# Kernel optimization log

Measured on AMD Instinct MI355X. Metric: run time of the kernel, lower is better.

## Reference

```python
import jax, jax.numpy as jnp
import numpy as np

N_NODES = 100000
FEAT = 256
HID = 256
BATCH = 512
NUM_SAMPLES = [25, 10]  # layer_infos[0].num_samples, layer_infos[1].num_samples


def setup_inputs() -> dict:
    key = jax.random.key(0)
    ks = jax.random.split(key, 7)
    scale = 0.05
    return {
        "features": jax.random.normal(ks[0], (N_NODES, FEAT), dtype=jnp.float32),
        "adj": jax.random.randint(ks[1], (N_NODES, NUM_SAMPLES[0]), 0, N_NODES, dtype=jnp.int32),
        "batch": jax.random.randint(ks[2], (BATCH,), 0, N_NODES, dtype=jnp.int32),
        "W_self_0": jax.random.normal(ks[3], (FEAT, HID), dtype=jnp.float32) * scale,
        "W_neigh_0": jax.random.normal(ks[4], (FEAT, HID), dtype=jnp.float32) * scale,
        "W_self_1": jax.random.normal(ks[5], (HID, HID), dtype=jnp.float32) * scale,
        "W_neigh_1": jax.random.normal(ks[6], (HID, HID), dtype=jnp.float32) * scale,
    }


def reference(features, adj, batch, W_self_0, W_neigh_0, W_self_1, W_neigh_1):
    B = batch.shape[0]
    n_layers = 2
    # --- sample(): reverse-order neighbor expansion (deterministic: first-k slots) ---
    # hop 1 uses layer_infos[-1].num_samples = 10, hop 2 uses layer_infos[0].num_samples = 25
    s1 = adj[batch][:, : NUM_SAMPLES[1]].reshape(-1)  # [B*10]
    s2 = adj[s1][:, : NUM_SAMPLES[0]].reshape(-1)     # [B*250]
    support = [1, NUM_SAMPLES[1], NUM_SAMPLES[1] * NUM_SAMPLES[0]]  # [1, 10, 250]
    # --- gather input features per hop (irregular gather, memory bound) ---
    hidden = [features[batch], features[s1], features[s2]]
    Ws = [(W_self_0, W_neigh_0), (W_self_1, W_neigh_1)]
    for layer in range(n_layers):
        act = jax.nn.relu if layer < n_layers - 1 else (lambda x: x)
        W_s, W_n = Ws[layer]
        next_hidden = []
        for hop in range(n_layers - layer):
            n_smp = NUM_SAMPLES[n_layers - hop - 1]
            self_vecs = hidden[hop]  # [B*support[hop], d]
            neigh = hidden[hop + 1].reshape(B * support[hop], n_smp, -1)
            neigh_mean = neigh.mean(axis=1)  # mean aggregator
            # concat=False -> sum of self and neighbor transforms
            next_hidden.append(act(self_vecs @ W_s + neigh_mean @ W_n))
        hidden = next_hidden
    out = hidden[0]  # [B, HID]
    # GraphSAGE l2-normalizes final embeddings
    norm = jnp.maximum(jnp.linalg.norm(out, axis=1, keepdims=True), 1e-12)
    return out / norm
```

## Files before the change

### kernel.cpp

```cpp
#include <hip/hip_runtime.h>
#include <cstdint>
#include <cstddef>

#define NNODES 100000
#define FEATD  256
#define HIDD   256
#define NBATCH 512
#define FAN1   10
#define FAN2   25
#define NS1    (NBATCH*FAN1)
#define MTOT   (NBATCH+NS1)

typedef __attribute__((ext_vector_type(8))) short short8;
typedef __attribute__((ext_vector_type(4))) float f32x4;

__device__ __forceinline__ unsigned short f2bf(float f) {
    unsigned int u = __float_as_uint(f);
    unsigned int r = (u + 0x7fffu + ((u >> 16) & 1u)) >> 16;
    return (unsigned short)r;
}
__device__ __forceinline__ float bf2f(unsigned short h) {
    return __uint_as_float(((unsigned int)h) << 16);
}

__global__ __launch_bounds__(256) void k_wcvt(
    const float* __restrict__ Ws0, const float* __restrict__ Wn0,
    const float* __restrict__ Ws1, const float* __restrict__ Wn1,
    unsigned short* __restrict__ B0t, unsigned short* __restrict__ B1t) {
    __shared__ unsigned short Ts[64][72];
    const int t     = threadIdx.x;
    const int which = blockIdx.x >> 5;
    const int loc   = blockIdx.x & 31;
    const int kt = loc >> 2, nt = loc & 3;
    const int k0 = kt * 64, n0 = nt * 64;
    const float* W;
    if (which == 0)
        W = (k0 < 256) ? (Ws0 + (size_t)k0 * 256) : (Wn0 + (size_t)(k0 - 256) * 256);
    else
        W = (k0 < 256) ? (Ws1 + (size_t)k0 * 256) : (Wn1 + (size_t)(k0 - 256) * 256);
    unsigned short* Bt = which ? B1t : B0t;
    #pragma unroll
    for (int i = 0; i < 4; ++i) {
        int s  = t + i * 256;
        int kr = s >> 4;
        int c4 = s & 15;
        float4 v = *reinterpret_cast<const float4*>(W + (size_t)kr * 256 + n0 + c4 * 4);
        Ts[c4 * 4 + 0][kr] = f2bf(v.x);
        Ts[c4 * 4 + 1][kr] = f2bf(v.y);
        Ts[c4 * 4 + 2][kr] = f2bf(v.z);
        Ts[c4 * 4 + 3][kr] = f2bf(v.w);
    }
    __syncthreads();
    #pragma unroll
    for (int i = 0; i < 2; ++i) {
        int s  = t + i * 256;
        int nl = s >> 3;
        int k8 = (s & 7) * 8;
        *reinterpret_cast<short8*>(Bt + (size_t)(n0 + nl) * 512 + k0 + k8) =
            *reinterpret_cast<const short8*>(&Ts[nl][k8]);
    }
}

__global__ __launch_bounds__(256, 3) void k_gg0(
    const float* __restrict__ feat, const int* __restrict__ adj,
    const int* __restrict__ batch, const unsigned short* __restrict__ B0t,
    unsigned short* __restrict__ H0, unsigned short* __restrict__ H1) {
    __shared__ __align__(16) unsigned short As[16][520];
    const int t   = threadIdx.x;
    const int wv  = t >> 6;
    const int l   = t & 63;
    const int q   = l >> 4;
    const int m15 = l & 15;
    const int r0  = blockIdx.x * 16;
    const bool isBatch = (r0 < NBATCH);

    #pragma unroll
    for (int i = 0; i < 4; ++i) {
        const int r = wv * 4 + i;
        const int R = r0 + r;
        int node;
        if (isBatch) {
            node = batch[R];
        } else {
            int idx = R - NBATCH;
            int b   = idx / FAN1;
            int j   = idx - b * FAN1;
            node = adj[(size_t)batch[b] * FAN2 + j];
        }
        float4 selfv = *reinterpret_cast<const float4*>(
            feat + (size_t)node * FEATD + l * 4);
        const int* arow = adj + (size_t)node * FAN2;
        int myidx = (l < FAN2) ? arow[l] : 0;
        float4 acc = make_float4(0.f, 0.f, 0.f, 0.f);
        float s;
        if (isBatch) {
            #pragma unroll
            for (int k = 0; k < FAN1; ++k) {
                int nb = __shfl(myidx, k);
                float4 v = *reinterpret_cast<const float4*>(
                    feat + (size_t)nb * FEATD + l * 4);
                acc.x += v.x; acc.y += v.y; acc.z += v.z; acc.w += v.w;
            }
            s = 1.0f / (float)FAN1;
        } else {
            #pragma unroll
            for (int k = 0; k < FAN2; ++k) {
                int nb = __shfl(myidx, k);
                float4 v = *reinterpret_cast<const float4*>(
                    feat + (size_t)nb * FEATD + l * 4);
                acc.x += v.x; acc.y += v.y; acc.z += v.z; acc.w += v.w;
            }
            s = 1.0f / (float)FAN2;
        }
        acc.x *= s; acc.y *= s; acc.z *= s; acc.w *= s;
        ushort4 ps, pn;
        ps.x = f2bf(selfv.x); ps.y = f2bf(selfv.y);
        ps.z = f2bf(selfv.z); ps.w = f2bf(selfv.w);
        pn.x = f2bf(acc.x);   pn.y = f2bf(acc.y);
        pn.z = f2bf(acc.z);   pn.w = f2bf(acc.w);
        *reinterpret_cast<ushort4*>(&As[r][l * 4])       = ps;
        *reinterpret_cast<ushort4*>(&As[r][256 + l * 4]) = pn;
    }
    __syncthreads();

    f32x4 acc0 = (f32x4)0.f, acc1 = (f32x4)0.f, acc2 = (f32x4)0.f, acc3 = (f32x4)0.f;
    const unsigned short* b0p = B0t + (size_t)(wv * 64 +  0 + m15) * 512;
    const unsigned short* b1p = B0t + (size_t)(wv * 64 + 16 + m15) * 512;
    const unsigned short* b2p = B0t + (size_t)(wv * 64 + 32 + m15) * 512;
    const unsigned short* b3p = B0t + (size_t)(wv * 64 + 48 + m15) * 512;
    #pragma unroll
    for (int kt = 0; kt < 16; ++kt) {
        const int kk = kt * 32 + q * 8;
        short8 a  = *reinterpret_cast<const short8*>(&As[m15][kk]);
        short8 b0 = *reinterpret_cast<const short8*>(b0p + kk);
        short8 b1 = *reinterpret_cast<const short8*>(b1p + kk);
        short8 b2 = *reinterpret_cast<const short8*>(b2p + kk);
        short8 b3 = *reinterpret_cast<const short8*>(b3p + kk);
        acc0 = __builtin_amdgcn_mfma_f32_16x16x32_bf16(a, b0, acc0, 0, 0, 0);
        acc1 = __builtin_amdgcn_mfma_f32_16x16x32_bf16(a, b1, acc1, 0, 0, 0);
        acc2 = __builtin_amdgcn_mfma_f32_16x16x32_bf16(a, b2, acc2, 0, 0, 0);
        acc3 = __builtin_amdgcn_mfma_f32_16x16x32_bf16(a, b3, acc3, 0, 0, 0);
    }

    #pragma unroll
    for (int f = 0; f < 4; ++f) {
        const int n = wv * 64 + f * 16 + m15;
        const f32x4& a = (f == 0) ? acc0 : (f == 1) ? acc1 : (f == 2) ? acc2 : acc3;
        #pragma unroll
        for (int j = 0; j < 4; ++j) {
            int m = r0 + q * 4 + j;
            unsigned short v = f2bf(fmaxf(a[j], 0.f));
            if (isBatch)
                H0[(size_t)m * HIDD + n] = v;
            else
                H1[(size_t)(m - NBATCH) * HIDD + n] = v;
        }
    }
}

__global__ __launch_bounds__(512) void k_l1(
    const unsigned short* __restrict__ H0, const unsigned short* __restrict__ H1,
    const unsigned short* __restrict__ B1t, float* __restrict__ out) {
    __shared__ __align__(16) unsigned short As[16][520];
    __shared__ float rn[16][8];
    const int t   = threadIdx.x;
    const int wv  = t >> 6;
    const int l   = t & 63;
    const int q   = l >> 4;
    const int m15 = l & 15;
    const int rb  = blockIdx.x * 16;

    {
        int r = t >> 5, c8 = (t & 31) * 8;
        *reinterpret_cast<short8*>(&As[r][c8]) =
            *reinterpret_cast<const short8*>(H0 + (size_t)(rb + r) * HIDD + c8);
    }
    {
        int r = t >> 5, c8 = (t & 31) * 8;
        const unsigned short* base = H1 + (size_t)(rb + r) * FAN1 * HIDD + c8;
        float a[8];
        #pragma unroll
        for (int e = 0; e < 8; ++e) a[e] = 0.f;
        #pragma unroll
        for (int j = 0; j < FAN1; ++j) {
            short8 v = *reinterpret_cast<const short8*>(base + (size_t)j * HIDD);
            #pragma unroll
            for (int e = 0; e < 8; ++e) a[e] += bf2f((unsigned short)v[e]);
        }
        short8 p;
        #pragma unroll
        for (int e = 0; e < 8; ++e) p[e] = (short)f2bf(a[e] * (1.0f / FAN1));
        *reinterpret_cast<short8*>(&As[r][256 + c8]) = p;
    }
    __syncthreads();

    f32x4 acc0 = (f32x4)0.f, acc1 = (f32x4)0.f;
    const unsigned short* b0p = B1t + (size_t)(wv * 32 + m15) * 512;
    const unsigned short* b1p = B1t + (size_t)(wv * 32 + 16 + m15) * 512;
    #pragma unroll
    for (int kt = 0; kt < 8; ++kt) {
        const int kb = kt * 64;
        #pragma unroll
        for (int s2 = 0; s2 < 2; ++s2) {
            const int kk = kb + s2 * 32 + q * 8;
            short8 a  = *reinterpret_cast<const short8*>(&As[m15][kk]);
            short8 b0 = *reinterpret_cast<const short8*>(b0p + kk);
            short8 b1 = *reinterpret_cast<const short8*>(b1p + kk);
            acc0 = __builtin_amdgcn_mfma_f32_16x16x32_bf16(a, b0, acc0, 0, 0, 0);
            acc1 = __builtin_amdgcn_mfma_f32_16x16x32_bf16(a, b1, acc1, 0, 0, 0);
        }
    }

    #pragma unroll
    for (int j = 0; j < 4; ++j) {
        float p = acc0[j] * acc0[j] + acc1[j] * acc1[j];
        p += __shfl_xor(p, 1);
        p += __shfl_xor(p, 2);
        p += __shfl_xor(p, 4);
        p += __shfl_xor(p, 8);
        if (m15 == 0) rn[q * 4 + j][wv] = p;
    }
    __syncthreads();

    #pragma unroll
    for (int j = 0; j < 4; ++j) {
        const int m = q * 4 + j;
        float s = rn[m][0] + rn[m][1] + rn[m][2] + rn[m][3]
                + rn[m][4] + rn[m][5] + rn[m][6] + rn[m][7];
        float inv = 1.0f / fmaxf(sqrtf(s), 1e-12f);
        out[(size_t)(rb + m) * HIDD + wv * 32 + m15]      = acc0[j] * inv;
        out[(size_t)(rb + m) * HIDD + wv * 32 + 16 + m15] = acc1[j] * inv;
    }
}

extern "C" void kernel_launch(void* const* d_in, const int* in_sizes, int n_in,
                              void* d_out, int out_size, void* d_ws, size_t ws_size,
                              hipStream_t stream) {
    const float* feat  = (const float*)d_in[0];
    const int*   adj   = (const int*)d_in[1];
    const int*   batch = (const int*)d_in[2];
    const float* Ws0   = (const float*)d_in[3];
    const float* Wn0   = (const float*)d_in[4];
    const float* Ws1   = (const float*)d_in[5];
    const float* Wn1   = (const float*)d_in[6];
    float* out = (float*)d_out;

    char* ws = (char*)d_ws;
    unsigned short* B0t = (unsigned short*)(ws + 0);
    unsigned short* B1t = (unsigned short*)(ws + 262144);
    unsigned short* H0  = (unsigned short*)(ws + 524288);
    unsigned short* H1  = (unsigned short*)(ws + 786432);

    k_wcvt<<<64, 256, 0, stream>>>(Ws0, Wn0, Ws1, Wn1, B0t, B1t);
    k_gg0<<<MTOT / 16, 256, 0, stream>>>(feat, adj, batch, B0t, H0, H1);
    k_l1<<<NBATCH / 16, 512, 0, stream>>>(H0, H1, B1t, out);
}
```

Measured before the change: 193.9 us.

## Fuse weight conversion, layer-0 gather-GEMM and layer-1 into one persistent kernel

After: 257.4 us. 32.8% more time.

```diff
diff --git a/kernel.cpp b/kernel.cpp
--- a/kernel.cpp
+++ b/kernel.cpp
@@ -10,6 +10,9 @@
 #define FAN2   25
 #define NS1    (NBATCH*FAN1)
 #define MTOT   (NBATCH+NS1)
+#define NBLK   (MTOT/16)
+#define NHOP   (NS1/16)
+#define CBASE  NHOP
 
 typedef __attribute__((ext_vector_type(8))) short short8;
 typedef __attribute__((ext_vector_type(4))) float f32x4;
@@ -23,69 +26,83 @@
     return __uint_as_float(((unsigned int)h) << 16);
 }
 
-__global__ __launch_bounds__(256) void k_wcvt(
+__device__ __forceinline__ void wait_flag(int* p, int target) {
+    while (__hip_atomic_load(p, __ATOMIC_ACQUIRE, __HIP_MEMORY_SCOPE_AGENT) < target)
+        __builtin_amdgcn_s_sleep(2);
+}
+
+__global__ void k_zero(int* __restrict__ f) {
+    if (threadIdx.x < 33) f[threadIdx.x] = 0;
+}
+
+__global__ __launch_bounds__(256, 3) void k_fused(
+    const float* __restrict__ feat, const int* __restrict__ adj,
+    const int* __restrict__ batch,
     const float* __restrict__ Ws0, const float* __restrict__ Wn0,
     const float* __restrict__ Ws1, const float* __restrict__ Wn1,
-    unsigned short* __restrict__ B0t, unsigned short* __restrict__ B1t) {
+    unsigned short* __restrict__ B0t, unsigned short* __restrict__ B1t,
+    unsigned short* __restrict__ H0, unsigned short* __restrict__ H1,
+    int* __restrict__ flags, float* __restrict__ out) {
     __shared__ unsigned short Ts[64][72];
-    const int t     = threadIdx.x;
-    const int which = blockIdx.x >> 5;
-    const int loc   = blockIdx.x & 31;
-    const int kt = loc >> 2, nt = loc & 3;
-    const int k0 = kt * 64, n0 = nt * 64;
-    const float* W;
-    if (which == 0)
-        W = (k0 < 256) ? (Ws0 + (size_t)k0 * 256) : (Wn0 + (size_t)(k0 - 256) * 256);
-    else
-        W = (k0 < 256) ? (Ws1 + (size_t)k0 * 256) : (Wn1 + (size_t)(k0 - 256) * 256);
-    unsigned short* Bt = which ? B1t : B0t;
-    #pragma unroll
-    for (int i = 0; i < 4; ++i) {
-        int s  = t + i * 256;
-        int kr = s >> 4;
-        int c4 = s & 15;
-        float4 v = *reinterpret_cast<const float4*>(W + (size_t)kr * 256 + n0 + c4 * 4);
-        Ts[c4 * 4 + 0][kr] = f2bf(v.x);
-        Ts[c4 * 4 + 1][kr] = f2bf(v.y);
-        Ts[c4 * 4 + 2][kr] = f2bf(v.z);
-        Ts[c4 * 4 + 3][kr] = f2bf(v.w);
-    }
-    __syncthreads();
-    #pragma unroll
-    for (int i = 0; i < 2; ++i) {
-        int s  = t + i * 256;
-        int nl = s >> 3;
-        int k8 = (s & 7) * 8;
-        *reinterpret_cast<short8*>(Bt + (size_t)(n0 + nl) * 512 + k0 + k8) =
-            *reinterpret_cast<const short8*>(&Ts[nl][k8]);
-    }
-}
-
-__global__ __launch_bounds__(256, 3) void k_gg0(
-    const float* __restrict__ feat, const int* __restrict__ adj,
-    const int* __restrict__ batch, const unsigned short* __restrict__ B0t,
-    unsigned short* __restrict__ H0, unsigned short* __restrict__ H1) {
     __shared__ __align__(16) unsigned short As[16][520];
+    __shared__ float rn[16][4];
     const int t   = threadIdx.x;
+    const int bid = blockIdx.x;
     const int wv  = t >> 6;
     const int l   = t & 63;
     const int q   = l >> 4;
     const int m15 = l & 15;
-    const int r0  = blockIdx.x * 16;
-    const bool isBatch = (r0 < NBATCH);
-
+    const bool isHop = (bid < NHOP);
+
+    if (bid < 64) {
+        const int which = bid >> 5;
+        const int loc   = bid & 31;
+        const int kt = loc >> 2, nt = loc & 3;
+        const int k0 = kt * 64, n0 = nt * 64;
+        const float* W;
+        if (which == 0)
+            W = (k0 < 256) ? (Ws0 + (size_t)k0 * 256) : (Wn0 + (size_t)(k0 - 256) * 256);
+        else
+            W = (k0 < 256) ? (Ws1 + (size_t)k0 * 256) : (Wn1 + (size_t)(k0 - 256) * 256);
+        unsigned short* Bt = which ? B1t : B0t;
+        #pragma unroll
+        for (int i = 0; i < 4; ++i) {
+            int s  = t + i * 256;
+            int kr = s >> 4;
+            int c4 = s & 15;
+            float4 v = *reinterpret_cast<const float4*>(W + (size_t)kr * 256 + n0 + c4 * 4);
+            Ts[c4 * 4 + 0][kr] = f2bf(v.x);
+            Ts[c4 * 4 + 1][kr] = f2bf(v.y);
+            Ts[c4 * 4 + 2][kr] = f2bf(v.z);
+            Ts[c4 * 4 + 3][kr] = f2bf(v.w);
+        }
+        __syncthreads();
+        #pragma unroll
+        for (int i = 0; i < 2; ++i) {
+            int s  = t + i * 256;
+            int nl = s >> 3;
+            int k8 = (s & 7) * 8;
+            *reinterpret_cast<short8*>(Bt + (size_t)(n0 + nl) * 512 + k0 + k8) =
+                *reinterpret_cast<const short8*>(&Ts[nl][k8]);
+        }
+        __threadfence();
+        __syncthreads();
+        if (t == 0)
+            __hip_atomic_fetch_add(&flags[0], 1, __ATOMIC_RELEASE, __HIP_MEMORY_SCOPE_AGENT);
+    }
+
+    const int rbase = isHop ? bid * 16 : (bid - CBASE) * 16;
     #pragma unroll
     for (int i = 0; i < 4; ++i) {
-        const int r = wv * 4 + i;
-        const int R = r0 + r;
+        const int r   = wv * 4 + i;
+        const int idx = rbase + r;
         int node;
-        if (isBatch) {
-            node = batch[R];
+        if (isHop) {
+            int b = idx / FAN1;
+            int j = idx - b * FAN1;
+            node  = adj[(size_t)batch[b] * FAN2 + j];
         } else {
-            int idx = R - NBATCH;
-            int b   = idx / FAN1;
-            int j   = idx - b * FAN1;
-            node = adj[(size_t)batch[b] * FAN2 + j];
+            node = batch[idx];
         }
         float4 selfv = *reinterpret_cast<const float4*>(
             feat + (size_t)node * FEATD + l * 4);
@@ -93,7 +110,16 @@
         int myidx = (l < FAN2) ? arow[l] : 0;
         float4 acc = make_float4(0.f, 0.f, 0.f, 0.f);
         float s;
-        if (isBatch) {
+        if (isHop) {
+            #pragma unroll
+            for (int k = 0; k < FAN2; ++k) {
+                int nb = __shfl(myidx, k);
+                float4 v = *reinterpret_cast<const float4*>(
+                    feat + (size_t)nb * FEATD + l * 4);
+                acc.x += v.x; acc.y += v.y; acc.z += v.z; acc.w += v.w;
+            }
+            s = 1.0f / (float)FAN2;
+        } else {
             #pragma unroll
             for (int k = 0; k < FAN1; ++k) {
                 int nb = __shfl(myidx, k);
@@ -102,15 +128,6 @@
                 acc.x += v.x; acc.y += v.y; acc.z += v.z; acc.w += v.w;
             }
             s = 1.0f / (float)FAN1;
-        } else {
-            #pragma unroll
-            for (int k = 0; k < FAN2; ++k) {
-                int nb = __shfl(myidx, k);
-                float4 v = *reinterpret_cast<const float4*>(
-                    feat + (size_t)nb * FEATD + l * 4);
-                acc.x += v.x; acc.y += v.y; acc.z += v.z; acc.w += v.w;
-            }
-            s = 1.0f / (float)FAN2;
         }
         acc.x *= s; acc.y *= s; acc.z *= s; acc.w *= s;
         ushort4 ps, pn;
@@ -123,11 +140,91 @@
     }
     __syncthreads();
 
+    if (t == 0) wait_flag(&flags[0], 64);
+    __syncthreads();
+
+    {
+        f32x4 acc0 = (f32x4)0.f, acc1 = (f32x4)0.f, acc2 = (f32x4)0.f, acc3 = (f32x4)0.f;
+        const unsigned short* b0p = B0t + (size_t)(wv * 64 +  0 + m15) * 512;
+        const unsigned short* b1p = B0t + (size_t)(wv * 64 + 16 + m15) * 512;
+        const unsigned short* b2p = B0t + (size_t)(wv * 64 + 32 + m15) * 512;
+        const unsigned short* b3p = B0t + (size_t)(wv * 64 + 48 + m15) * 512;
+        #pragma unroll
+        for (int kt = 0; kt < 16; ++kt) {
+            const int kk = kt * 32 + q * 8;
+            short8 a  = *reinterpret_cast<const short8*>(&As[m15][kk]);
+            short8 b0 = *reinterpret_cast<const short8*>(b0p + kk);
+            short8 b1 = *reinterpret_cast<const short8*>(b1p + kk);
+            short8 b2 = *reinterpret_cast<const short8*>(b2p + kk);
+            short8 b3 = *reinterpret_cast<const short8*>(b3p + kk);
+            acc0 = __builtin_amdgcn_mfma_f32_16x16x32_bf16(a, b0, acc0, 0, 0, 0);
+            acc1 = __builtin_amdgcn_mfma_f32_16x16x32_bf16(a, b1, acc1, 0, 0, 0);
+            acc2 = __builtin_amdgcn_mfma_f32_16x16x32_bf16(a, b2, acc2, 0, 0, 0);
+            acc3 = __builtin_amdgcn_mfma_f32_16x16x32_bf16(a, b3, acc3, 0, 0, 0);
+        }
+        #pragma unroll
+        for (int f = 0; f < 4; ++f) {
+            const int n = wv * 64 + f * 16 + m15;
+            const f32x4& a = (f == 0) ? acc0 : (f == 1) ? acc1 : (f == 2) ? acc2 : acc3;
+            #pragma unroll
+            for (int j = 0; j < 4; ++j) {
+                int m = rbase + q * 4 + j;
+                unsigned short v = f2bf(fmaxf(a[j], 0.f));
+                if (isHop)
+                    H1[(size_t)m * HIDD + n] = v;
+                else
+                    H0[(size_t)m * HIDD + n] = v;
+            }
+        }
+    }
+    __threadfence();
+    __syncthreads();
+
+    if (isHop) {
+        if (t == 0)
+            __hip_atomic_fetch_add(&flags[1 + bid / 10], 1,
+                                   __ATOMIC_RELEASE, __HIP_MEMORY_SCOPE_AGENT);
+        return;
+    }
+
+    const int g  = bid - CBASE;
+    const int rb = rbase;
+    if (t == 0) wait_flag(&flags[1 + g], 10);
+    __syncthreads();
+
+    #pragma unroll
+    for (int i = 0; i < 2; ++i) {
+        int s = t + i * 256;
+        int r = s >> 5, c8 = (s & 31) * 8;
+        *reinterpret_cast<short8*>(&As[r][c8]) =
+            *reinterpret_cast<const short8*>(H0 + (size_t)(rb + r) * HIDD + c8);
+    }
+    #pragma unroll
+    for (int i = 0; i < 2; ++i) {
+        int s = t + i * 256;
+        int r = s >> 5, c8 = (s & 31) * 8;
+        const unsigned short* base = H1 + (size_t)(rb + r) * FAN1 * HIDD + c8;
+        float a[8];
+        #pragma unroll
+        for (int e = 0; e < 8; ++e) a[e] = 0.f;
+        #pragma unroll
+        for (int j = 0; j < FAN1; ++j) {
+            short8 v = *reinterpret_cast<const short8*>(base + (size_t)j * HIDD);
+            #pragma unroll
+            for (int e = 0; e < 8; ++e) a[e] += bf2f((unsigned short)v[e]);
+        }
+        short8 p;
+        #pragma unroll
+        for (int e = 0; e < 8; ++e) p[e] = (short)f2bf(a[e] * (1.0f / FAN1));
+        *reinterpret_cast<short8*>(&As[r][256 + c8]) = p;
+    }
+    __syncthreads();
+
     f32x4 acc0 = (f32x4)0.f, acc1 = (f32x4)0.f, acc2 = (f32x4)0.f, acc3 = (f32x4)0.f;
-    const unsigned short* b0p = B0t + (size_t)(wv * 64 +  0 + m15) * 512;
-    const unsigned short* b1p = B0t + (size_t)(wv * 64 + 16 + m15) * 512;
-    const unsigned short* b2p = B0t + (size_t)(wv * 64 + 32 + m15) * 512;
-    const unsigned short* b3p = B0t + (size_t)(wv * 64 + 48 + m15) * 512;
+    const unsigned short* b0p = B1t + (size_t)(wv * 64 +  0 + m15) * 512;
+    const unsigned short* b1p = B1t + (size_t)(wv * 64 + 16 + m15) * 512;
+    const unsigned short* b2p = B1t + (size_t)(wv * 64 + 32 + m15) * 512;
+    const unsigned short* b3p = B1t + (size_t)(wv * 64 + 48 + m15) * 512;
     #pragma unroll
     for (int kt = 0; kt < 16; ++kt) {
         const int kk = kt * 32 + q * 8;
@@ -143,77 +240,9 @@
     }
 
     #pragma unroll
-    for (int f = 0; f < 4; ++f) {
-        const int n = wv * 64 + f * 16 + m15;
-        const f32x4& a = (f == 0) ? acc0 : (f == 1) ? acc1 : (f == 2) ? acc2 : acc3;
-        #pragma unroll
-        for (int j = 0; j < 4; ++j) {
-            int m = r0 + q * 4 + j;
-            unsigned short v = f2bf(fmaxf(a[j], 0.f));
-            if (isBatch)
-                H0[(size_t)m * HIDD + n] = v;
-            else
-                H1[(size_t)(m - NBATCH) * HIDD + n] = v;
-        }
-    }
-}
-
-__global__ __launch_bounds__(512) void k_l1(
-    const unsigned short* __restrict__ H0, const unsigned short* __restrict__ H1,
-    const unsigned short* __restrict__ B1t, float* __restrict__ out) {
-    __shared__ __align__(16) unsigned short As[16][520];
-    __shared__ float rn[16][8];
-    const int t   = threadIdx.x;
-    const int wv  = t >> 6;
-    const int l   = t & 63;
-    const int q   = l >> 4;
-    const int m15 = l & 15;
-    const int rb  = blockIdx.x * 16;
-
-    {
-        int r = t >> 5, c8 = (t & 31) * 8;
-        *reinterpret_cast<short8*>(&As[r][c8]) =
-            *reinterpret_cast<const short8*>(H0 + (size_t)(rb + r) * HIDD + c8);
-    }
-    {
-        int r = t >> 5, c8 = (t & 31) * 8;
-        const unsigned short* base = H1 + (size_t)(rb + r) * FAN1 * HIDD + c8;
-        float a[8];
-        #pragma unroll
-        for (int e = 0; e < 8; ++e) a[e] = 0.f;
-        #pragma unroll
-        for (int j = 0; j < FAN1; ++j) {
-            short8 v = *reinterpret_cast<const short8*>(base + (size_t)j * HIDD);
-            #pragma unroll
-            for (int e = 0; e < 8; ++e) a[e] += bf2f((unsigned short)v[e]);
-        }
-        short8 p;
-        #pragma unroll
-        for (int e = 0; e < 8; ++e) p[e] = (short)f2bf(a[e] * (1.0f / FAN1));
-        *reinterpret_cast<short8*>(&As[r][256 + c8]) = p;
-    }
-    __syncthreads();
-
-    f32x4 acc0 = (f32x4)0.f, acc1 = (f32x4)0.f;
-    const unsigned short* b0p = B1t + (size_t)(wv * 32 + m15) * 512;
-    const unsigned short* b1p = B1t + (size_t)(wv * 32 + 16 + m15) * 512;
-    #pragma unroll
-    for (int kt = 0; kt < 8; ++kt) {
-        const int kb = kt * 64;
-        #pragma unroll
-        for (int s2 = 0; s2 < 2; ++s2) {
-            const int kk = kb + s2 * 32 + q * 8;
-            short8 a  = *reinterpret_cast<const short8*>(&As[m15][kk]);
-            short8 b0 = *reinterpret_cast<const short8*>(b0p + kk);
-            short8 b1 = *reinterpret_cast<const short8*>(b1p + kk);
-            acc0 = __builtin_amdgcn_mfma_f32_16x16x32_bf16(a, b0, acc0, 0, 0, 0);
-            acc1 = __builtin_amdgcn_mfma_f32_16x16x32_bf16(a, b1, acc1, 0, 0, 0);
-        }
-    }
-
-    #pragma unroll
     for (int j = 0; j < 4; ++j) {
-        float p = acc0[j] * acc0[j] + acc1[j] * acc1[j];
+        float p = acc0[j] * acc0[j] + acc1[j] * acc1[j]
+                + acc2[j] * acc2[j] + acc3[j] * acc3[j];
         p += __shfl_xor(p, 1);
         p += __shfl_xor(p, 2);
         p += __shfl_xor(p, 4);
@@ -225,11 +254,12 @@
     #pragma unroll
     for (int j = 0; j < 4; ++j) {
         const int m = q * 4 + j;
-        float s = rn[m][0] + rn[m][1] + rn[m][2] + rn[m][3]
-                + rn[m][4] + rn[m][5] + rn[m][6] + rn[m][7];
+        float s = rn[m][0] + rn[m][1] + rn[m][2] + rn[m][3];
         float inv = 1.0f / fmaxf(sqrtf(s), 1e-12f);
-        out[(size_t)(rb + m) * HIDD + wv * 32 + m15]      = acc0[j] * inv;
-        out[(size_t)(rb + m) * HIDD + wv * 32 + 16 + m15] = acc1[j] * inv;
+        out[(size_t)(rb + m) * HIDD + wv * 64 +  0 + m15] = acc0[j] * inv;
+        out[(size_t)(rb + m) * HIDD + wv * 64 + 16 + m15] = acc1[j] * inv;
+        out[(size_t)(rb + m) * HIDD + wv * 64 + 32 + m15] = acc2[j] * inv;
+        out[(size_t)(rb + m) * HIDD + wv * 64 + 48 + m15] = acc3[j] * inv;
     }
 }
 
@@ -250,8 +280,9 @@
     unsigned short* B1t = (unsigned short*)(ws + 262144);
     unsigned short* H0  = (unsigned short*)(ws + 524288);
     unsigned short* H1  = (unsigned short*)(ws + 786432);
-
-    k_wcvt<<<64, 256, 0, stream>>>(Ws0, Wn0, Ws1, Wn1, B0t, B1t);
-    k_gg0<<<MTOT / 16, 256, 0, stream>>>(feat, adj, batch, B0t, H0, H1);
-    k_l1<<<NBATCH / 16, 512, 0, stream>>>(H0, H1, B1t, out);
-}
+    int*            flg = (int*)(ws + 3407872);
+
+    k_zero<<<1, 64, 0, stream>>>(flg);
+    k_fused<<<NBLK, 256, 0, stream>>>(feat, adj, batch, Ws0, Wn0, Ws1, Wn1,
+                                      B0t, B1t, H0, H1, flg, out);
+}
```
